# Kernel tuning notes

Hardware: AMD Instinct MI355X
Metric: run time of the kernel (lower is better)

Reference implementation:

```python
import jax, jax.numpy as jnp
import numpy as np
from jax import lax

B, C, H, W = 4, 64, 128, 128
G, K, RED = 16, 7, 4        # groups, kernel size, reduce ratio
CR = C // RED               # reduced channels for kernel generation
EPS = 1e-5                  # BatchNorm eps (torch default)
DN = ('NCHW', 'OIHW', 'NCHW')


def setup_inputs() -> dict:
    key = jax.random.key(0)
    ks = jax.random.split(key, 5)
    return {
        'input': jax.random.normal(ks[0], (B, C, H, W), jnp.float32),
        # initial_mapping: depthwise 3x3 conv + pointwise 1x1 conv (bias=False)
        'w_dw': jax.random.normal(ks[1], (C, 1, 3, 3), jnp.float32) * 0.1,
        'w_pw': jax.random.normal(ks[2], (C, C), jnp.float32) * (1.0 / np.sqrt(C)),
        # sigma_mapping BatchNorm affine params
        'bn_gamma': jnp.ones((CR,), jnp.float32),
        'bn_beta': jnp.zeros((CR,), jnp.float32),
        # reduce / span 1x1 convs (bias=False)
        'w_reduce': jax.random.normal(ks[3], (CR, C), jnp.float32) * (1.0 / np.sqrt(C)),
        'w_span': jax.random.normal(ks[4], (K * K * G, CR), jnp.float32) * (1.0 / np.sqrt(CR)),
    }


def reference(input, w_dw, w_pw, bn_gamma, bn_beta, w_reduce, w_span):
    x = input
    # initial mapping: depthwise 3x3 (pad 1) then 1x1 pointwise
    h = lax.conv_general_dilated(x, w_dw, (1, 1), [(1, 1), (1, 1)],
                                 feature_group_count=C, dimension_numbers=DN)
    h = jnp.einsum('bchw,oc->bohw', h, w_pw)
    # unfold -> [B, C*K*K, H, W] with channel-major feature ordering (matches torch Unfold)
    patches = lax.conv_general_dilated_patches(h, (K, K), (1, 1), [(3, 3), (3, 3)],
                                               dimension_numbers=DN)
    patches = patches.reshape(B, G, C // G, K * K, H, W)
    # kernel generation: o_mapping is identity (stride 1 avg pool), then reduce -> BN(train) -> ReLU -> span
    r = jnp.einsum('bchw,oc->bohw', x, w_reduce)           # [B, CR, H, W]
    mean = r.mean(axis=(0, 2, 3), keepdims=True)
    var = r.var(axis=(0, 2, 3), keepdims=True)             # biased var, as torch BN training
    r = (r - mean) * lax.rsqrt(var + EPS) * bn_gamma[None, :, None, None] + bn_beta[None, :, None, None]
    r = jax.nn.relu(r)
    kern = jnp.einsum('bchw,oc->bohw', r, w_span)          # [B, G*K*K, H, W]
    kern = kern.reshape(B, G, 1, K * K, H, W)
    out = (kern * patches).sum(axis=3)                     # [B, G, C//G, H, W]
    return out.reshape(B, C, H, W)
```

## Files before the change

kernel.cpp:

```cpp
#include <hip/hip_runtime.h>

typedef _Float16 half2v __attribute__((ext_vector_type(2)));
typedef _Float16 half4v __attribute__((ext_vector_type(4)));
typedef _Float16 half8v __attribute__((ext_vector_type(8)));
typedef float f32x4 __attribute__((ext_vector_type(4)));

__launch_bounds__(256, 4)
__global__ void k_front(const float* __restrict__ in, const float* __restrict__ wdw,
                        const float* __restrict__ wpw, const float* __restrict__ wred,
                        const float* __restrict__ wspan,
                        _Float16* __restrict__ h16, _Float16* __restrict__ r16,
                        float* __restrict__ stats, _Float16* __restrict__ w16){
  __shared__ float4 s_in4[4][10][12];
  __shared__ __attribute__((aligned(16))) _Float16 s_dwh[64][72];
  __shared__ __attribute__((aligned(16))) _Float16 s_cvh[64][72];
  __shared__ float s_red[4][32];
  int t = threadIdx.x;
  int w = t >> 6, lane = t & 63;
  int lx = lane & 7, ly = lane >> 3;
  int c15 = lane & 15, hi = lane >> 4;
  int blk0 = blockIdx.x;

  {
    int i = blk0 * 256 + t;
    if (i < 12544) w16[i] = (_Float16)wspan[i];
  }

  int blk = ((blk0 & 7) << 7) | (blk0 >> 3);
  int tile = blk & 255, b = blk >> 8;
  int x0 = (tile & 15) << 3, y0 = (tile >> 4) << 3;
  const float* inb = in + ((long)b << 20) + ((long)(w << 2) << 14);

  const float* ap = wpw + (((w << 4) + c15) << 6) + (hi << 3);
  float4 ap0 = *(const float4*)(ap);
  float4 ap1 = *(const float4*)(ap + 4);
  float4 ap2 = *(const float4*)(ap + 32);
  float4 ap3 = *(const float4*)(ap + 36);
  const float* arp = wred + (c15 << 6) + (hi << 3);
  float4 ar0 = *(const float4*)(arp);
  float4 ar1 = *(const float4*)(arp + 4);
  float4 ar2 = *(const float4*)(arp + 32);
  float4 ar3 = *(const float4*)(arp + 36);
  half8v a_pw0 = {(_Float16)ap0.x,(_Float16)ap0.y,(_Float16)ap0.z,(_Float16)ap0.w,
                  (_Float16)ap1.x,(_Float16)ap1.y,(_Float16)ap1.z,(_Float16)ap1.w};
  half8v a_pw1 = {(_Float16)ap2.x,(_Float16)ap2.y,(_Float16)ap2.z,(_Float16)ap2.w,
                  (_Float16)ap3.x,(_Float16)ap3.y,(_Float16)ap3.z,(_Float16)ap3.w};
  half8v a_rd0 = {(_Float16)ar0.x,(_Float16)ar0.y,(_Float16)ar0.z,(_Float16)ar0.w,
                  (_Float16)ar1.x,(_Float16)ar1.y,(_Float16)ar1.z,(_Float16)ar1.w};
  half8v a_rd1 = {(_Float16)ar2.x,(_Float16)ar2.y,(_Float16)ar2.z,(_Float16)ar2.w,
                  (_Float16)ar3.x,(_Float16)ar3.y,(_Float16)ar3.z,(_Float16)ar3.w};

  int p1 = lane + 64;
  int ry0 = lane / 10, rx0 = lane - ry0 * 10;
  int ry1 = p1 / 10,   rx1 = p1 - ry1 * 10;
  int yy0 = y0 + ry0 - 1, xx0 = x0 + rx0 - 1;
  int yy1 = y0 + ry1 - 1, xx1 = x0 + rx1 - 1;
  bool ok0 = (unsigned)yy0 < 128u && (unsigned)xx0 < 128u;
  bool ok1 = (p1 < 100) && ((unsigned)yy1 < 128u) && ((unsigned)xx1 < 128u);
  int o0 = (yy0 << 7) + xx0, o1 = (yy1 << 7) + xx1;

  float4 v0 = make_float4(0.f,0.f,0.f,0.f), v1 = make_float4(0.f,0.f,0.f,0.f);
  if (ok0){ v0.x = inb[o0]; v0.y = inb[o0+16384]; v0.z = inb[o0+32768]; v0.w = inb[o0+49152]; }
  if (ok1){ v1.x = inb[o1]; v1.y = inb[o1+16384]; v1.z = inb[o1+32768]; v1.w = inb[o1+49152]; }

  for (int q = 0; q < 4; q++){
    s_in4[w][ry0][rx0] = v0;
    if (p1 < 100) s_in4[w][ry1][rx1] = v1;
    __builtin_amdgcn_wave_barrier();

    if (q < 3){
      const float* pq = inb + ((long)(q + 1) << 18);
      v0 = make_float4(0.f,0.f,0.f,0.f); v1 = make_float4(0.f,0.f,0.f,0.f);
      if (ok0){ v0.x = pq[o0]; v0.y = pq[o0+16384]; v0.z = pq[o0+32768]; v0.w = pq[o0+49152]; }
      if (ok1){ v1.x = pq[o1]; v1.y = pq[o1+16384]; v1.z = pq[o1+32768]; v1.w = pq[o1+49152]; }
    }

    int wdbase = __builtin_amdgcn_readfirstlane(((q << 4) + (w << 2)) * 9);
    const float* wd = wdw + wdbase;
    float4 a = make_float4(0.f,0.f,0.f,0.f);
    float4 cv = make_float4(0.f,0.f,0.f,0.f);
    #pragma unroll
    for (int dy = 0; dy < 3; dy++){
      #pragma unroll
      for (int dx = 0; dx < 3; dx++){
        float4 v = s_in4[w][ly + dy][lx + dx];
        int k = dy * 3 + dx;
        a.x += v.x * wd[k];
        a.y += v.y * wd[9 + k];
        a.z += v.z * wd[18 + k];
        a.w += v.w * wd[27 + k];
        if (k == 4) cv = v;
      }
    }
    int cb = (q << 4) + (w << 2);
    half4v ah = {(_Float16)a.x,(_Float16)a.y,(_Float16)a.z,(_Float16)a.w};
    half4v eh = {(_Float16)cv.x,(_Float16)cv.y,(_Float16)cv.z,(_Float16)cv.w};
    *(half4v*)&s_dwh[lane][cb] = ah;
    *(half4v*)&s_cvh[lane][cb] = eh;
  }

  __syncthreads();

  f32x4 z = {0.f,0.f,0.f,0.f};
  f32x4 acc[4] = {z, z, z, z};
  #pragma unroll
  for (int tt = 0; tt < 4; tt++){
    half8v b0 = *(const half8v*)&s_dwh[(tt << 4) + c15][hi << 3];
    half8v b1 = *(const half8v*)&s_dwh[(tt << 4) + c15][32 + (hi << 3)];
    acc[tt] = __builtin_amdgcn_mfma_f32_16x16x32_f16(a_pw0, b0, acc[tt], 0, 0, 0);
    acc[tt] = __builtin_amdgcn_mfma_f32_16x16x32_f16(a_pw1, b1, acc[tt], 0, 0, 0);
  }
  #pragma unroll
  for (int tt = 0; tt < 4; tt++){
    int px = (tt << 4) + c15;
    int pyl = px >> 3, pxl = px & 7;
    int gout = (w << 2) + hi;
    long off = ((((long)((b << 4) + gout)) << 14) + ((y0 + pyl) << 7) + x0 + pxl) << 2;
    half4v hv = {(_Float16)acc[tt][0], (_Float16)acc[tt][1],
                 (_Float16)acc[tt][2], (_Float16)acc[tt][3]};
    *(half4v*)&h16[off] = hv;
  }

  f32x4 rac = z;
  {
    half8v b0 = *(const half8v*)&s_cvh[(w << 4) + c15][hi << 3];
    half8v b1 = *(const half8v*)&s_cvh[(w << 4) + c15][32 + (hi << 3)];
    rac = __builtin_amdgcn_mfma_f32_16x16x32_f16(a_rd0, b0, rac, 0, 0, 0);
    rac = __builtin_amdgcn_mfma_f32_16x16x32_f16(a_rd1, b1, rac, 0, 0, 0);
  }
  {
    int px = (w << 4) + c15;
    int pyl = px >> 3, pxl = px & 7;
    long roff = ((((long)b << 14) + ((y0 + pyl) << 7) + x0 + pxl) << 4) + (hi << 2);
    half4v rv4 = {(_Float16)rac[0], (_Float16)rac[1], (_Float16)rac[2], (_Float16)rac[3]};
    *(half4v*)&r16[roff] = rv4;
  }

  #pragma unroll
  for (int rr = 0; rr < 4; rr++){
    float v = rac[rr], s2 = v * v;
    #pragma unroll
    for (int m = 1; m < 16; m <<= 1){
      v  += __shfl_xor(v,  m, 64);
      s2 += __shfl_xor(s2, m, 64);
    }
    if (c15 == 0){
      int ch = (hi << 2) + rr;
      s_red[w][2 * ch]     = v;
      s_red[w][2 * ch + 1] = s2;
    }
  }
  __syncthreads();
  if (t < 32){
    float sum = s_red[0][t] + s_red[1][t] + s_red[2][t] + s_red[3][t];
    atomicAdd(&stats[t], sum);
  }
}

__launch_bounds__(256)
__global__ void k_main(const _Float16* __restrict__ h16, const _Float16* __restrict__ r16,
                       const float* __restrict__ stats, const float* __restrict__ gamma,
                       const float* __restrict__ beta, const _Float16* __restrict__ w16,
                       float* __restrict__ out){
  __shared__ float4 s_h4[22][24];
  __shared__ float  s_sb[32];
  int t = threadIdx.x;
  int g = blockIdx.y, b = blockIdx.z;
  int bx = blockIdx.x;
  bx = ((bx & 7) << 3) | (bx >> 3);
  int tx0 = (bx & 7) << 4, ty0 = (bx >> 3) << 4;

  int ltx = t & 15, lty = t >> 4;
  int px = tx0 + ltx, py = ty0 + lty;

  const _Float16* rp = r16 + ((((long)b << 14) + (py << 7) + px) << 4);
  half8v ra = *(const half8v*)rp;
  half8v rb = *(const half8v*)(rp + 8);

  const _Float16* hp = h16 + (((long)((b << 4) + g)) << 16);
  for (int p = t; p < 484; p += 256){
    int ry = p / 22, rx = p - ry * 22;
    int yy = ty0 + ry - 3, xx = tx0 + rx - 3;
    float4 v = make_float4(0.f,0.f,0.f,0.f);
    if ((unsigned)yy < 128u && (unsigned)xx < 128u){
      half4v hh = *(const half4v*)&hp[(long)(((yy << 7) + xx) << 2)];
      v = make_float4((float)hh[0], (float)hh[1], (float)hh[2], (float)hh[3]);
    }
    s_h4[ry][rx] = v;
  }

  if (t < 16){
    const float inv_n = 1.52587890625e-5f;
    float mean = stats[2 * t] * inv_n;
    float var  = stats[2 * t + 1] * inv_n - mean * mean;
    float inv  = rsqrtf(var + 1e-5f);
    float sc   = gamma[t] * inv;
    s_sb[2 * t]     = sc;
    s_sb[2 * t + 1] = beta[t] - mean * sc;
  }
  __syncthreads();

  float rv[16];
  #pragma unroll
  for (int c = 0; c < 8; c++){
    rv[c]     = fmaxf((float)ra[c] * s_sb[2*c]     + s_sb[2*c+1],     0.f);
    rv[c + 8] = fmaxf((float)rb[c] * s_sb[2*(c+8)] + s_sb[2*(c+8)+1], 0.f);
  }
#if __has_builtin(__builtin_amdgcn_fdot2)
  half2v rv2[8];
  #pragma unroll
  for (int j = 0; j < 8; j++){
    half2v pk; pk[0] = (_Float16)rv[2*j]; pk[1] = (_Float16)rv[2*j+1];
    rv2[j] = pk;
  }
#endif

  const _Float16* wg = w16 + g * 784;
#if __has_builtin(__builtin_amdgcn_fdot2)
  const half2v* wg2 = (const half2v*)wg;
#endif
  float acc0 = 0.f, acc1 = 0.f, acc2 = 0.f, acc3 = 0.f;
  #pragma unroll
  for (int kh = 0; kh < 7; kh++){
    #pragma unroll
    for (int kw = 0; kw < 7; kw++){
      int k = kh * 7 + kw;
      float kv0 = 0.f, kv1 = 0.f;
#if __has_builtin(__builtin_amdgcn_fdot2)
      #pragma unroll
      for (int j = 0; j < 4; j++){
        kv0 = __builtin_amdgcn_fdot2(rv2[j],     wg2[k*8 + j],     kv0, false);
        kv1 = __builtin_amdgcn_fdot2(rv2[j + 4], wg2[k*8 + j + 4], kv1, false);
      }
#else
      #pragma unroll
      for (int c = 0; c < 8; c++){
        kv0 += rv[c]     * (float)wg[k*16 + c];
        kv1 += rv[c + 8] * (float)wg[k*16 + c + 8];
      }
#endif
      float kv = kv0 + kv1;
      float4 hv = s_h4[lty + kh][ltx + kw];
      acc0 += kv * hv.x;
      acc1 += kv * hv.y;
      acc2 += kv * hv.z;
      acc3 += kv * hv.w;
    }
  }

  long obase = (((long)((b << 6) + (g << 2))) << 14) + (py << 7) + px;
  out[obase]         = acc0;
  out[obase + 16384] = acc1;
  out[obase + 32768] = acc2;
  out[obase + 49152] = acc3;
}

extern "C" void kernel_launch(void* const* d_in, const int* in_sizes, int n_in,
                              void* d_out, int out_size, void* d_ws, size_t ws_size,
                              hipStream_t stream){
  const float* in       = (const float*)d_in[0];
  const float* w_dw     = (const float*)d_in[1];
  const float* w_pw     = (const float*)d_in[2];
  const float* gamma    = (const float*)d_in[3];
  const float* beta     = (const float*)d_in[4];
  const float* w_reduce = (const float*)d_in[5];
  const float* w_span   = (const float*)d_in[6];
  float* out = (float*)d_out;

  _Float16* h16 = (_Float16*)d_ws;
  _Float16* r16 = h16 + 4194304;
  _Float16* w16 = r16 + 1048576;
  float* stats  = (float*)(w16 + 12544);

  hipMemsetAsync(stats, 0, 32 * sizeof(float), stream);
  k_front<<<1024, 256, 0, stream>>>(in, w_dw, w_pw, w_reduce, w_span,
                                    h16, r16, stats, w16);
  dim3 grid(64, 16, 4);
  k_main <<<grid, 256, 0, stream>>>(h16, r16, stats, gamma, beta, w16, out);
}
```

Before: 125.1 us.

## Replace stats atomics with partial-sum reduction kernel and process two tiles per block

k_front now writes per-block partial BN sums instead of atomically adding into global stats, and a new single-block k_red kernel reduces them and precomputes the BN scale and bias, which also removes the memset. k_main now handles two horizontally adjacent 16x16 tiles per block, prefetching the second tile's halo into registers while computing the first, and its launch bounds add an occupancy hint of 6. This trades an extra kernel launch and a serial reduction for no atomic contention, and trades more register pressure and extra syncs for better latency hiding. A leftover dead loop computes values that are never used.

```diff
diff --git a/kernel.cpp b/kernel.cpp
--- a/kernel.cpp
+++ b/kernel.cpp
@@ -10,7 +10,7 @@
                         const float* __restrict__ wpw, const float* __restrict__ wred,
                         const float* __restrict__ wspan,
                         _Float16* __restrict__ h16, _Float16* __restrict__ r16,
-                        float* __restrict__ stats, _Float16* __restrict__ w16){
+                        float* __restrict__ partial, _Float16* __restrict__ w16){
   __shared__ float4 s_in4[4][10][12];
   __shared__ __attribute__((aligned(16))) _Float16 s_dwh[64][72];
   __shared__ __attribute__((aligned(16))) _Float16 s_cvh[64][72];
@@ -151,108 +151,172 @@
     }
   }
   __syncthreads();
+  if (t < 32)
+    partial[(blk0 << 5) + t] = s_red[0][t] + s_red[1][t] + s_red[2][t] + s_red[3][t];
+}
+
+__global__ void k_red(const float* __restrict__ partial, const float* __restrict__ gamma,
+                      const float* __restrict__ beta, float* __restrict__ sb){
+  __shared__ float sp[1024];
+  int t = threadIdx.x;
+  int c = t & 31, grp = t >> 5;
+  float s = 0.f;
+  #pragma unroll 4
+  for (int i = grp; i < 1024; i += 32) s += partial[(i << 5) + c];
+  sp[t] = s;
+  __syncthreads();
   if (t < 32){
-    float sum = s_red[0][t] + s_red[1][t] + s_red[2][t] + s_red[3][t];
-    atomicAdd(&stats[t], sum);
+    float v = 0.f;
+    #pragma unroll
+    for (int k = 0; k < 32; k++) v += sp[(k << 5) + t];
+    sp[t] = v;
+  }
+  __syncthreads();
+  if (t < 16){
+    const float inv_n = 1.52587890625e-5f;
+    float mean = sp[2 * t] * inv_n;
+    float var  = sp[2 * t + 1] * inv_n - mean * mean;
+    float inv  = rsqrtf(var + 1e-5f);
+    float sc   = gamma[t] * inv;
+    sb[2 * t]     = sc;
+    sb[2 * t + 1] = beta[t] - mean * sc;
   }
 }
 
-__launch_bounds__(256)
+__launch_bounds__(256, 6)
 __global__ void k_main(const _Float16* __restrict__ h16, const _Float16* __restrict__ r16,
-                       const float* __restrict__ stats, const float* __restrict__ gamma,
-                       const float* __restrict__ beta, const _Float16* __restrict__ w16,
+                       const float* __restrict__ sb, const _Float16* __restrict__ w16,
                        float* __restrict__ out){
   __shared__ float4 s_h4[22][24];
-  __shared__ float  s_sb[32];
   int t = threadIdx.x;
   int g = blockIdx.y, b = blockIdx.z;
-  int bx = blockIdx.x;
-  bx = ((bx & 7) << 3) | (bx >> 3);
-  int tx0 = (bx & 7) << 4, ty0 = (bx >> 3) << 4;
-
+  int t0 = blockIdx.x << 1;
   int ltx = t & 15, lty = t >> 4;
-  int px = tx0 + ltx, py = ty0 + lty;
-
-  const _Float16* rp = r16 + ((((long)b << 14) + (py << 7) + px) << 4);
-  half8v ra = *(const half8v*)rp;
-  half8v rb = *(const half8v*)(rp + 8);
+  int txA = (t0 & 7) << 4, ty0 = (t0 >> 3) << 4;
+  int txB = txA + 16;
+  int pxA = txA + ltx, py = ty0 + lty;
+
+  const _Float16* rpA = r16 + ((((long)b << 14) + (py << 7) + pxA) << 4);
+  half8v raA = *(const half8v*)rpA,         rbA = *(const half8v*)(rpA + 8);
+  half8v raB = *(const half8v*)(rpA + 256), rbB = *(const half8v*)(rpA + 264);
 
   const _Float16* hp = h16 + (((long)((b << 4) + g)) << 16);
-  for (int p = t; p < 484; p += 256){
-    int ry = p / 22, rx = p - ry * 22;
-    int yy = ty0 + ry - 3, xx = tx0 + rx - 3;
-    float4 v = make_float4(0.f,0.f,0.f,0.f);
-    if ((unsigned)yy < 128u && (unsigned)xx < 128u){
-      half4v hh = *(const half4v*)&hp[(long)(((yy << 7) + xx) << 2)];
-      v = make_float4((float)hh[0], (float)hh[1], (float)hh[2], (float)hh[3]);
-    }
-    s_h4[ry][rx] = v;
-  }
-
-  if (t < 16){
-    const float inv_n = 1.52587890625e-5f;
-    float mean = stats[2 * t] * inv_n;
-    float var  = stats[2 * t + 1] * inv_n - mean * mean;
-    float inv  = rsqrtf(var + 1e-5f);
-    float sc   = gamma[t] * inv;
-    s_sb[2 * t]     = sc;
-    s_sb[2 * t + 1] = beta[t] - mean * sc;
-  }
-  __syncthreads();
-
-  float rv[16];
-  #pragma unroll
-  for (int c = 0; c < 8; c++){
-    rv[c]     = fmaxf((float)ra[c] * s_sb[2*c]     + s_sb[2*c+1],     0.f);
-    rv[c + 8] = fmaxf((float)rb[c] * s_sb[2*(c+8)] + s_sb[2*(c+8)+1], 0.f);
-  }
+  int p1 = t + 256;
+  int ry0 = t / 22,  rx0 = t - ry0 * 22;
+  int ry1 = p1 / 22, rx1 = p1 - ry1 * 22;
+  int yy0 = ty0 + ry0 - 3, yy1 = ty0 + ry1 - 3;
+  bool oky0 = (unsigned)yy0 < 128u;
+  bool oky1 = (p1 < 484) && ((unsigned)yy1 < 128u);
+  int xA0 = txA + rx0 - 3, xA1 = txA + rx1 - 3;
+
+  half4v hA0 = {0,0,0,0}, hA1 = {0,0,0,0}, hB0 = {0,0,0,0}, hB1 = {0,0,0,0};
+  if (oky0 && (unsigned)xA0 < 128u) hA0 = *(const half4v*)&hp[(long)(((yy0 << 7) + xA0) << 2)];
+  if (oky1 && (unsigned)xA1 < 128u) hA1 = *(const half4v*)&hp[(long)(((yy1 << 7) + xA1) << 2)];
+  if (oky0 && (unsigned)(xA0 + 16) < 128u) hB0 = *(const half4v*)&hp[(long)(((yy0 << 7) + xA0 + 16) << 2)];
+  if (oky1 && (unsigned)(xA1 + 16) < 128u) hB1 = *(const half4v*)&hp[(long)(((yy1 << 7) + xA1 + 16) << 2)];
+
+  s_h4[ry0][rx0] = make_float4((float)hA0[0], (float)hA0[1], (float)hA0[2], (float)hA0[3]);
+  if (p1 < 484)
+    s_h4[ry1][rx1] = make_float4((float)hA1[0], (float)hA1[1], (float)hA1[2], (float)hA1[3]);
+
+  float scl[16], ofs[16];
+  #pragma unroll
+  for (int c = 0; c < 16; c++){ scl[c] = sb[2 * c]; ofs[c] = sb[2 * c + 1]; }
+
+  half2v rvA[8], rvB[8];
+  #pragma unroll
+  for (int j = 0; j < 8; j++){
+    float v0 = fmaxf((float)raA[j] * scl[j]     + ofs[j],     0.f);
+    float v1 = fmaxf((float)rbA[j] * scl[j + 8] + ofs[j + 8], 0.f);
+    (void)v0; (void)v1;
+  }
+  {
+    float rv[16];
+    #pragma unroll
+    for (int c = 0; c < 8; c++){
+      rv[c]     = fmaxf((float)raA[c] * scl[c]     + ofs[c],     0.f);
+      rv[c + 8] = fmaxf((float)rbA[c] * scl[c + 8] + ofs[c + 8], 0.f);
+    }
+    #pragma unroll
+    for (int j = 0; j < 8; j++){
+      half2v pk; pk[0] = (_Float16)rv[2 * j]; pk[1] = (_Float16)rv[2 * j + 1];
+      rvA[j] = pk;
+    }
+  }
+
+  const _Float16* wg = w16 + g * 784;
+  const half2v* wg2 = (const half2v*)wg;
+
+  float aA0 = 0.f, aA1 = 0.f, aA2 = 0.f, aA3 = 0.f;
+  float aB0 = 0.f, aB1 = 0.f, aB2 = 0.f, aB3 = 0.f;
+
+  auto run49 = [&](const half2v (&rv2)[8], float& a0, float& a1, float& a2, float& a3){
+    #pragma unroll
+    for (int kh = 0; kh < 7; kh++){
+      #pragma unroll
+      for (int kw = 0; kw < 7; kw++){
+        int k = kh * 7 + kw;
+        float kv0 = 0.f, kv1 = 0.f;
 #if __has_builtin(__builtin_amdgcn_fdot2)
-  half2v rv2[8];
-  #pragma unroll
-  for (int j = 0; j < 8; j++){
-    half2v pk; pk[0] = (_Float16)rv[2*j]; pk[1] = (_Float16)rv[2*j+1];
-    rv2[j] = pk;
-  }
+        #pragma unroll
+        for (int j = 0; j < 4; j++){
+          kv0 = __builtin_amdgcn_fdot2(rv2[j],     wg2[k * 8 + j],     kv0, false);
+          kv1 = __builtin_amdgcn_fdot2(rv2[j + 4], wg2[k * 8 + j + 4], kv1, false);
+        }
+#else
+        #pragma unroll
+        for (int j = 0; j < 4; j++){
+          kv0 += (float)rv2[j][0]     * (float)wg2[k * 8 + j][0]
+               + (float)rv2[j][1]     * (float)wg2[k * 8 + j][1];
+          kv1 += (float)rv2[j + 4][0] * (float)wg2[k * 8 + j + 4][0]
+               + (float)rv2[j + 4][1] * (float)wg2[k * 8 + j + 4][1];
+        }
 #endif
-
-  const _Float16* wg = w16 + g * 784;
-#if __has_builtin(__builtin_amdgcn_fdot2)
-  const half2v* wg2 = (const half2v*)wg;
-#endif
-  float acc0 = 0.f, acc1 = 0.f, acc2 = 0.f, acc3 = 0.f;
-  #pragma unroll
-  for (int kh = 0; kh < 7; kh++){
-    #pragma unroll
-    for (int kw = 0; kw < 7; kw++){
-      int k = kh * 7 + kw;
-      float kv0 = 0.f, kv1 = 0.f;
-#if __has_builtin(__builtin_amdgcn_fdot2)
-      #pragma unroll
-      for (int j = 0; j < 4; j++){
-        kv0 = __builtin_amdgcn_fdot2(rv2[j],     wg2[k*8 + j],     kv0, false);
-        kv1 = __builtin_amdgcn_fdot2(rv2[j + 4], wg2[k*8 + j + 4], kv1, false);
+        float kv = kv0 + kv1;
+        float4 hv = s_h4[lty + kh][ltx + kw];
+        a0 += kv * hv.x;
+        a1 += kv * hv.y;
+        a2 += kv * hv.z;
+        a3 += kv * hv.w;
       }
-#else
-      #pragma unroll
-      for (int c = 0; c < 8; c++){
-        kv0 += rv[c]     * (float)wg[k*16 + c];
-        kv1 += rv[c + 8] * (float)wg[k*16 + c + 8];
-      }
-#endif
-      float kv = kv0 + kv1;
-      float4 hv = s_h4[lty + kh][ltx + kw];
-      acc0 += kv * hv.x;
-      acc1 += kv * hv.y;
-      acc2 += kv * hv.z;
-      acc3 += kv * hv.w;
-    }
-  }
-
-  long obase = (((long)((b << 6) + (g << 2))) << 14) + (py << 7) + px;
-  out[obase]         = acc0;
-  out[obase + 16384] = acc1;
-  out[obase + 32768] = acc2;
-  out[obase + 49152] = acc3;
+    }
+  };
+
+  __syncthreads();
+  run49(rvA, aA0, aA1, aA2, aA3);
+  __syncthreads();
+
+  s_h4[ry0][rx0] = make_float4((float)hB0[0], (float)hB0[1], (float)hB0[2], (float)hB0[3]);
+  if (p1 < 484)
+    s_h4[ry1][rx1] = make_float4((float)hB1[0], (float)hB1[1], (float)hB1[2], (float)hB1[3]);
+
+  {
+    float rv[16];
+    #pragma unroll
+    for (int c = 0; c < 8; c++){
+      rv[c]     = fmaxf((float)raB[c] * scl[c]     + ofs[c],     0.f);
+      rv[c + 8] = fmaxf((float)rbB[c] * scl[c + 8] + ofs[c + 8], 0.f);
+    }
+    #pragma unroll
+    for (int j = 0; j < 8; j++){
+      half2v pk; pk[0] = (_Float16)rv[2 * j]; pk[1] = (_Float16)rv[2 * j + 1];
+      rvB[j] = pk;
+    }
+  }
+
+  __syncthreads();
+  run49(rvB, aB0, aB1, aB2, aB3);
+
+  long obA = (((long)((b << 6) + (g << 2))) << 14) + (py << 7) + pxA;
+  out[obA]         = aA0;
+  out[obA + 16384] = aA1;
+  out[obA + 32768] = aA2;
+  out[obA + 49152] = aA3;
+  long obB = obA + 16;
+  out[obB]         = aB0;
+  out[obB + 16384] = aB1;
+  out[obB + 32768] = aB2;
+  out[obB + 49152] = aB3;
 }
 
 extern "C" void kernel_launch(void* const* d_in, const int* in_sizes, int n_in,
@@ -270,11 +334,12 @@
   _Float16* h16 = (_Float16*)d_ws;
   _Float16* r16 = h16 + 4194304;
   _Float16* w16 = r16 + 1048576;
-  float* stats  = (float*)(w16 + 12544);
-
-  hipMemsetAsync(stats, 0, 32 * sizeof(float), stream);
+  float* partial = (float*)(w16 + 16384);
+  float* sb      = partial + 32768;
+
   k_front<<<1024, 256, 0, stream>>>(in, w_dw, w_pw, w_reduce, w_span,
-                                    h16, r16, stats, w16);
-  dim3 grid(64, 16, 4);
-  k_main <<<grid, 256, 0, stream>>>(h16, r16, stats, gamma, beta, w16, out);
+                                    h16, r16, partial, w16);
+  k_red  <<<1, 1024, 0, stream>>>(partial, gamma, beta, sb);
+  dim3 grid(32, 16, 4);
+  k_main <<<grid, 256, 0, stream>>>(h16, r16, sb, w16, out);
 }
```

After: 247.9 us. +98.2%, slower.

## Replace atomic BN stats with partials plus reduce kernel, deepen input prefetch

Applied to the files above, without the earlier changes.

The front kernel now writes per-block BN partial sums instead of issuing atomicAdds to a memset buffer. A new single-block kernel reduces those partials, computes the BN scale and bias once, and converts w_span to fp16. The main kernel just loads the precomputed scale and bias. The depthwise stage also prefetches two channel slices ahead using double register buffers. This drops the memset and the atomic contention, but adds an extra kernel launch, a serial single-block reduction, and more register pressure in k_front.

```diff
diff --git a/kernel.cpp b/kernel.cpp
--- a/kernel.cpp
+++ b/kernel.cpp
@@ -8,9 +8,8 @@
 __launch_bounds__(256, 4)
 __global__ void k_front(const float* __restrict__ in, const float* __restrict__ wdw,
                         const float* __restrict__ wpw, const float* __restrict__ wred,
-                        const float* __restrict__ wspan,
                         _Float16* __restrict__ h16, _Float16* __restrict__ r16,
-                        float* __restrict__ stats, _Float16* __restrict__ w16){
+                        float* __restrict__ partial){
   __shared__ float4 s_in4[4][10][12];
   __shared__ __attribute__((aligned(16))) _Float16 s_dwh[64][72];
   __shared__ __attribute__((aligned(16))) _Float16 s_cvh[64][72];
@@ -20,11 +19,6 @@
   int lx = lane & 7, ly = lane >> 3;
   int c15 = lane & 15, hi = lane >> 4;
   int blk0 = blockIdx.x;
-
-  {
-    int i = blk0 * 256 + t;
-    if (i < 12544) w16[i] = (_Float16)wspan[i];
-  }
 
   int blk = ((blk0 & 7) << 7) | (blk0 >> 3);
   int tile = blk & 255, b = blk >> 8;
@@ -59,22 +53,7 @@
   bool ok1 = (p1 < 100) && ((unsigned)yy1 < 128u) && ((unsigned)xx1 < 128u);
   int o0 = (yy0 << 7) + xx0, o1 = (yy1 << 7) + xx1;
 
-  float4 v0 = make_float4(0.f,0.f,0.f,0.f), v1 = make_float4(0.f,0.f,0.f,0.f);
-  if (ok0){ v0.x = inb[o0]; v0.y = inb[o0+16384]; v0.z = inb[o0+32768]; v0.w = inb[o0+49152]; }
-  if (ok1){ v1.x = inb[o1]; v1.y = inb[o1+16384]; v1.z = inb[o1+32768]; v1.w = inb[o1+49152]; }
-
-  for (int q = 0; q < 4; q++){
-    s_in4[w][ry0][rx0] = v0;
-    if (p1 < 100) s_in4[w][ry1][rx1] = v1;
-    __builtin_amdgcn_wave_barrier();
-
-    if (q < 3){
-      const float* pq = inb + ((long)(q + 1) << 18);
-      v0 = make_float4(0.f,0.f,0.f,0.f); v1 = make_float4(0.f,0.f,0.f,0.f);
-      if (ok0){ v0.x = pq[o0]; v0.y = pq[o0+16384]; v0.z = pq[o0+32768]; v0.w = pq[o0+49152]; }
-      if (ok1){ v1.x = pq[o1]; v1.y = pq[o1+16384]; v1.z = pq[o1+32768]; v1.w = pq[o1+49152]; }
-    }
-
+  auto dw_dep = [&](int q){
     int wdbase = __builtin_amdgcn_readfirstlane(((q << 4) + (w << 2)) * 9);
     const float* wd = wdw + wdbase;
     float4 a = make_float4(0.f,0.f,0.f,0.f);
@@ -97,6 +76,42 @@
     half4v eh = {(_Float16)cv.x,(_Float16)cv.y,(_Float16)cv.z,(_Float16)cv.w};
     *(half4v*)&s_dwh[lane][cb] = ah;
     *(half4v*)&s_cvh[lane][cb] = eh;
+  };
+
+  float4 vA0 = make_float4(0.f,0.f,0.f,0.f), vA1 = vA0, vB0 = vA0, vB1 = vA0;
+  if (ok0){ vA0.x = inb[o0]; vA0.y = inb[o0+16384]; vA0.z = inb[o0+32768]; vA0.w = inb[o0+49152]; }
+  if (ok1){ vA1.x = inb[o1]; vA1.y = inb[o1+16384]; vA1.z = inb[o1+32768]; vA1.w = inb[o1+49152]; }
+  {
+    const float* p1q = inb + (1L << 18);
+    if (ok0){ vB0.x = p1q[o0]; vB0.y = p1q[o0+16384]; vB0.z = p1q[o0+32768]; vB0.w = p1q[o0+49152]; }
+    if (ok1){ vB1.x = p1q[o1]; vB1.y = p1q[o1+16384]; vB1.z = p1q[o1+32768]; vB1.w = p1q[o1+49152]; }
+  }
+
+  #pragma unroll
+  for (int qq = 0; qq < 2; qq++){
+    s_in4[w][ry0][rx0] = vA0;
+    if (p1 < 100) s_in4[w][ry1][rx1] = vA1;
+    __builtin_amdgcn_wave_barrier();
+    if (qq == 0){
+      const float* pq = inb + (2L << 18);
+      vA0 = make_float4(0.f,0.f,0.f,0.f); vA1 = vA0;
+      if (ok0){ vA0.x = pq[o0]; vA0.y = pq[o0+16384]; vA0.z = pq[o0+32768]; vA0.w = pq[o0+49152]; }
+      if (ok1){ vA1.x = pq[o1]; vA1.y = pq[o1+16384]; vA1.z = pq[o1+32768]; vA1.w = pq[o1+49152]; }
+    }
+    dw_dep(qq << 1);
+    __builtin_amdgcn_wave_barrier();
+
+    s_in4[w][ry0][rx0] = vB0;
+    if (p1 < 100) s_in4[w][ry1][rx1] = vB1;
+    __builtin_amdgcn_wave_barrier();
+    if (qq == 0){
+      const float* pq = inb + (3L << 18);
+      vB0 = make_float4(0.f,0.f,0.f,0.f); vB1 = vB0;
+      if (ok0){ vB0.x = pq[o0]; vB0.y = pq[o0+16384]; vB0.z = pq[o0+32768]; vB0.w = pq[o0+49152]; }
+      if (ok1){ vB1.x = pq[o1]; vB1.y = pq[o1+16384]; vB1.z = pq[o1+32768]; vB1.w = pq[o1+49152]; }
+    }
+    dw_dep((qq << 1) + 1);
+    __builtin_amdgcn_wave_barrier();
   }
 
   __syncthreads();
@@ -151,16 +166,43 @@
     }
   }
   __syncthreads();
+  if (t < 32)
+    partial[(blk0 << 5) + t] = s_red[0][t] + s_red[1][t] + s_red[2][t] + s_red[3][t];
+}
+
+__global__ void k_red(const float* __restrict__ partial, const float* __restrict__ gamma,
+                      const float* __restrict__ beta, float* __restrict__ sb,
+                      const float* __restrict__ wspan, _Float16* __restrict__ w16){
+  __shared__ float sp[1024];
+  int t = threadIdx.x;
+  int c = t & 31, grp = t >> 5;
+  float s = 0.f;
+  #pragma unroll 4
+  for (int i = grp; i < 1024; i += 32) s += partial[(i << 5) + c];
+  sp[t] = s;
+  for (int i = t; i < 12544; i += 1024) w16[i] = (_Float16)wspan[i];
+  __syncthreads();
   if (t < 32){
-    float sum = s_red[0][t] + s_red[1][t] + s_red[2][t] + s_red[3][t];
-    atomicAdd(&stats[t], sum);
+    float v = 0.f;
+    #pragma unroll
+    for (int k = 0; k < 32; k++) v += sp[(k << 5) + t];
+    sp[t] = v;
+  }
+  __syncthreads();
+  if (t < 16){
+    const float inv_n = 1.52587890625e-5f;
+    float mean = sp[2 * t] * inv_n;
+    float var  = sp[2 * t + 1] * inv_n - mean * mean;
+    float inv  = rsqrtf(var + 1e-5f);
+    float sc   = gamma[t] * inv;
+    sb[2 * t]     = sc;
+    sb[2 * t + 1] = beta[t] - mean * sc;
   }
 }
 
 __launch_bounds__(256)
 __global__ void k_main(const _Float16* __restrict__ h16, const _Float16* __restrict__ r16,
-                       const float* __restrict__ stats, const float* __restrict__ gamma,
-                       const float* __restrict__ beta, const _Float16* __restrict__ w16,
+                       const float* __restrict__ sb, const _Float16* __restrict__ w16,
                        float* __restrict__ out){
   __shared__ float4 s_h4[22][24];
   __shared__ float  s_sb[32];
@@ -188,16 +230,7 @@
     }
     s_h4[ry][rx] = v;
   }
-
-  if (t < 16){
-    const float inv_n = 1.52587890625e-5f;
-    float mean = stats[2 * t] * inv_n;
-    float var  = stats[2 * t + 1] * inv_n - mean * mean;
-    float inv  = rsqrtf(var + 1e-5f);
-    float sc   = gamma[t] * inv;
-    s_sb[2 * t]     = sc;
-    s_sb[2 * t + 1] = beta[t] - mean * sc;
-  }
+  if (t < 32) s_sb[t] = sb[t];
   __syncthreads();
 
   float rv[16];
@@ -270,11 +303,11 @@
   _Float16* h16 = (_Float16*)d_ws;
   _Float16* r16 = h16 + 4194304;
   _Float16* w16 = r16 + 1048576;
-  float* stats  = (float*)(w16 + 12544);
-
-  hipMemsetAsync(stats, 0, 32 * sizeof(float), stream);
-  k_front<<<1024, 256, 0, stream>>>(in, w_dw, w_pw, w_reduce, w_span,
-                                    h16, r16, stats, w16);
+  float* partial = (float*)(w16 + 16384);
+  float* sb      = partial + 32768;
+
+  k_front<<<1024, 256, 0, stream>>>(in, w_dw, w_pw, w_reduce, h16, r16, partial);
+  k_red  <<<1, 1024, 0, stream>>>(partial, gamma, beta, sb, w_span, w16);
   dim3 grid(64, 16, 4);
-  k_main <<<grid, 256, 0, stream>>>(h16, r16, stats, gamma, beta, w16, out);
+  k_main <<<grid, 256, 0, stream>>>(h16, r16, sb, w16, out);
 }
```

Result: no change. 122.8 us (-1.9%).
